# Optimization experiments

Hardware: AMD Instinct MI355X
Metric: run time of the kernel (lower is better)

The kernel has to match this reference:

```python
import jax, jax.numpy as jnp
from jax import lax
import numpy as np

EPS = 0.1          # DBSCAN radius (init arg eps)
MIN_SAMPLES = 5    # DBSCAN min_samples (init arg min_samples)
NC_MAX = 512       # fixed padded cluster budget (8 per dim * 64 dims)


def _dbscan_1d(x):
    """Exact 1-D DBSCAN on a vector x of shape (N,).
    Returns (labels, n_clusters). labels[i] in [-1, n_clusters), -1 = noise.
    Clusters are numbered in ascending value order (canonical deterministic
    relabeling of sklearn's discovery order). Border points are attached to
    the nearest core point (ties -> left)."""
    n = x.shape[0]
    order = jnp.argsort(x)
    xs = x[order]
    # core test: #points within [xs-eps, xs+eps] >= min_samples
    hi = jnp.searchsorted(xs, xs + EPS, side='right')
    lo = jnp.searchsorted(xs, xs - EPS, side='left')
    core = (hi - lo) >= MIN_SAMPLES
    inf = jnp.inf
    core_vals = jnp.where(core, xs, -inf)
    run_max = lax.cummax(core_vals, axis=0)                 # nearest core value to the left (incl self)
    prev_core_val = jnp.concatenate([jnp.full((1,), -inf, xs.dtype), run_max[:-1]])
    # a core point starts a new cluster iff no core point within eps on its left
    new_cluster = core & ((xs - prev_core_val) > EPS)
    starts = jnp.cumsum(new_cluster.astype(jnp.int32))
    cid = starts - 1                                        # cluster id carried along sorted order
    ncl = starts[-1]
    # nearest core on the left / right (values and their cluster ids)
    left_cid = lax.cummax(jnp.where(core, cid, -1), axis=0)
    left_val = run_max
    right_cid = lax.cummin(jnp.where(core, cid, n + 1), axis=0, reverse=True)
    right_val = lax.cummin(jnp.where(core, xs, inf), axis=0, reverse=True)
    dl = xs - left_val
    dr = right_val - xs
    border_cid = jnp.where(dl <= dr, left_cid, right_cid)
    border_ok = jnp.minimum(dl, dr) <= EPS
    lab_sorted = jnp.where(core, cid, jnp.where(border_ok, border_cid, -1))
    labels = jnp.zeros_like(lab_sorted).at[order].set(lab_sorted)  # unsort to original node order
    return labels, ncl


def setup_inputs() -> dict:
    key = jax.random.key(0)
    features = jax.random.normal(key, (8, 16384, 64), dtype=jnp.float32)
    return {"features": features}


def reference(features):
    B, N, D = features.shape
    xt = jnp.transpose(features, (0, 2, 1))                  # (B, D, N)
    labels, ncl = jax.vmap(jax.vmap(_dbscan_1d))(xt)         # (B, D, N), (B, D)
    off = jnp.cumsum(ncl, axis=1) - ncl                      # exclusive prefix: global cluster offset per dim
    glb = jnp.where(labels >= 0, labels + off[:, :, None], -1)
    # noise / overflow -> dump into padding column NC_MAX, sliced off below
    lbl = jnp.where(glb >= 0, jnp.minimum(glb, NC_MAX), NC_MAX)
    inc = jnp.zeros((B, N, NC_MAX + 1), features.dtype)
    b_ix = jnp.arange(B)[:, None, None]
    n_ix = jnp.arange(N)[None, None, :]
    inc = inc.at[b_ix, n_ix, lbl].set(1.0)                   # scatter cluster membership
    return inc[:, :, :NC_MAX]                                # (B, N, NC_MAX) padded incidence matrix
```

## Files before the change

kernel.cpp:

```cpp
#include <hip/hip_runtime.h>

#define NPTS   16384
#define NDIM   64
#define NBATCH 8
#define TB     1024
#define VPT    16
#define NB     8192
#define BPT    8
#define EPSF   0.1f
#define MINS   5
#define NCMAX  512
#define BIGI   0x3fffffff

__device__ __forceinline__ int phys(int i)  { return i ^ ((i >> 5) & 15); }
__device__ __forceinline__ int lphys(int i) { return i ^ (((i >> 6) & 31) << 1); }

__device__ __forceinline__ int binof(float x, float mn, float inv) {
  float fb = (x - mn) * inv;
  int b = (int)fb;
  if (fb < 0.f) b = 0;
  if (b > NB - 1) b = NB - 1;
  return b;
}

__global__ void ktrans(const float* __restrict__ f, float* __restrict__ xt) {
  __shared__ float tile[64][65];
  int blk = blockIdx.x;
  int b   = blk >> 8;
  int n0  = (blk & 255) << 6;
  for (int i = threadIdx.x; i < 64 * 64; i += 256) {
    int n = i >> 6, d = i & 63;
    tile[n][d] = f[((size_t)b * NPTS + n0 + n) * NDIM + d];
  }
  __syncthreads();
  for (int i = threadIdx.x; i < 64 * 64; i += 256) {
    int d = i >> 6, n = i & 63;
    xt[((size_t)b * NDIM + d) * NPTS + n0 + n] = tile[n][d];
  }
}

struct FS { int h; float f; float l; int li; int c; };
__device__ __forceinline__ FS fsid() { FS r; r.h = 0; r.f = 0.f; r.l = 0.f; r.li = -1; r.c = 0; return r; }
__device__ __forceinline__ FS fscomb(FS a, FS b) {
  FS r;
  r.h  = a.h | b.h;
  r.f  = a.h ? a.f : b.f;
  r.l  = b.h ? b.l : a.l;
  r.li = b.h ? b.li : a.li;
  int gap = (a.h && b.h && ((b.f - a.l) > EPSF)) ? 1 : 0;
  r.c  = a.c + b.c + gap;
  return r;
}

__global__ void __launch_bounds__(TB) kdbscan(const float* __restrict__ xt,
                                              short* __restrict__ labels,
                                              int* __restrict__ nclg) {
  const int tid  = threadIdx.x;
  const int lane = tid & 63;
  const int wid  = tid >> 6;
  const int bd   = blockIdx.x;
  const float* __restrict__ x = xt + (size_t)bd * NPTS;

  __shared__ float xs[NPTS];
  __shared__ unsigned int hist[NB];
  __shared__ unsigned int offs[NB];
  __shared__ float wmn[16], wmx[16];
  __shared__ unsigned int wsum[16];
  __shared__ int   sh[16];  __shared__ float sf[16], sl[16];
  __shared__ int   sli[16]; __shared__ int   sc[16];
  __shared__ int   wri[16]; __shared__ float wrv[16];
  short* lab = (short*)hist;

  float v[VPT];
  float mn = INFINITY, mx = -INFINITY;
  #pragma unroll
  for (int s = 0; s < VPT; ++s) {
    v[s] = x[tid + s * TB];
    mn = fminf(mn, v[s]); mx = fmaxf(mx, v[s]);
  }
  for (int d = 1; d < 64; d <<= 1) {
    mn = fminf(mn, __shfl_xor(mn, d));
    mx = fmaxf(mx, __shfl_xor(mx, d));
  }
  if (lane == 0) { wmn[wid] = mn; wmx[wid] = mx; }
  __syncthreads();
  mn = wmn[0]; mx = wmx[0];
  for (int w = 1; w < 16; ++w) { mn = fminf(mn, wmn[w]); mx = fmaxf(mx, wmx[w]); }
  float range = mx - mn;
  float inv = (range > 0.f) ? ((float)NB / range) : 0.f;

  for (int i = tid; i < NB; i += TB) hist[i] = 0u;
  __syncthreads();
  #pragma unroll
  for (int s = 0; s < VPT; ++s) atomicAdd(&hist[binof(v[s], mn, inv)], 1u);
  __syncthreads();

  unsigned int loc[BPT];
  unsigned int run = 0;
  const int bbase = tid * BPT;
  #pragma unroll
  for (int j = 0; j < BPT; ++j) { loc[j] = run; run += hist[bbase + j]; }
  unsigned int incl = run;
  for (int d = 1; d < 64; d <<= 1) {
    unsigned int u = __shfl_up(incl, d);
    if (lane >= d) incl += u;
  }
  unsigned int exc = __shfl_up(incl, 1);
  if (lane == 0) exc = 0u;
  if (lane == 63) wsum[wid] = incl;
  __syncthreads();
  unsigned int wb = 0;
  for (int w = 0; w < wid; ++w) wb += wsum[w];
  unsigned int tb0 = wb + exc;
  #pragma unroll
  for (int j = 0; j < BPT; ++j) offs[bbase + j] = tb0 + loc[j];
  __syncthreads();

  int pos[VPT];
  #pragma unroll
  for (int s = 0; s < VPT; ++s) {
    int b = binof(v[s], mn, inv);
    int p = (int)atomicAdd(&offs[b], 1u);
    pos[s] = p;
    xs[phys(p)] = v[s];
  }
  __syncthreads();

  int tgt[VPT];
  #pragma unroll
  for (int s = 0; s < VPT; ++s) {
    int b  = binof(v[s], mn, inv);
    int e0 = (int)offs[b];
    int s0 = e0 - (int)hist[b];
    float vv = v[s]; int pp = pos[s];
    int r = 0;
    for (int j = s0; j < e0; ++j) {
      float xj = xs[phys(j)];
      r += (xj < vv || (xj == vv && j < pp)) ? 1 : 0;
    }
    tgt[s] = s0 + r;
  }
  __syncthreads();
  #pragma unroll
  for (int s = 0; s < VPT; ++s) xs[phys(tgt[s])] = v[s];
  __syncthreads();

  const int p0 = tid * VPT;
  float w[VPT + 8];
  #pragma unroll
  for (int k = 0; k < VPT + 8; ++k) {
    int i = p0 - 4 + k;
    w[k] = (i < 0) ? -INFINITY : ((i >= NPTS) ? INFINITY : xs[phys(i)]);
  }
  unsigned int coremask = 0u;
  #pragma unroll
  for (int s = 0; s < VPT; ++s) {
    float xi = w[s + 4];
    float lo = xi - EPSF, hi = xi + EPSF;
    bool core = false;
    #pragma unroll
    for (int t = 0; t < MINS; ++t)
      core |= (w[s + 4 - t] >= lo) && (w[s + 8 - t] <= hi);
    if (core) coremask |= (1u << s);
  }

  FS ch = fsid();
  #pragma unroll
  for (int s = 0; s < VPT; ++s) {
    if ((coremask >> s) & 1u) {
      float xv = w[s + 4];
      if (!ch.h) { ch.h = 1; ch.f = xv; }
      else if ((xv - ch.l) > EPSF) ++ch.c;
      ch.l = xv; ch.li = p0 + s;
    }
  }
  FS cur = ch;
  for (int d = 1; d < 64; d <<= 1) {
    FS u;
    u.h  = __shfl_up(cur.h, d);
    u.f  = __shfl_up(cur.f, d);
    u.l  = __shfl_up(cur.l, d);
    u.li = __shfl_up(cur.li, d);
    u.c  = __shfl_up(cur.c, d);
    FS cmb = fscomb(u, cur);
    if (lane >= d) cur = cmb;
  }
  FS exs;
  exs.h  = __shfl_up(cur.h, 1);
  exs.f  = __shfl_up(cur.f, 1);
  exs.l  = __shfl_up(cur.l, 1);
  exs.li = __shfl_up(cur.li, 1);
  exs.c  = __shfl_up(cur.c, 1);
  if (lane == 0) exs = fsid();
  if (lane == 63) { sh[wid] = cur.h; sf[wid] = cur.f; sl[wid] = cur.l; sli[wid] = cur.li; sc[wid] = cur.c; }
  __syncthreads();
  FS pre = fsid();
  for (int w2 = 0; w2 < wid; ++w2) {
    FS t; t.h = sh[w2]; t.f = sf[w2]; t.l = sl[w2]; t.li = sli[w2]; t.c = sc[w2];
    pre = fscomb(pre, t);
  }
  FS sp = fscomb(pre, exs);

  float P  = sp.h ? sp.l  : -INFINITY;
  int   Pi = sp.h ? sp.li : -1;
  int starts = sp.h ? (sp.c + 1) : 0;
  int   li[VPT];
  float lv[VPT];
  #pragma unroll
  for (int s = 0; s < VPT; ++s) {
    int i = p0 + s;
    if ((coremask >> s) & 1u) {
      float xv = w[s + 4];
      if ((xv - P) > EPSF) ++starts;
      P = xv; Pi = i;
      lab[lphys(i)] = (short)(starts - 1);
    }
    li[s] = Pi; lv[s] = P;
  }
  if (tid == TB - 1) nclg[bd] = starts;

  int fi_ = BIGI; float fv_ = 0.f;
  #pragma unroll
  for (int s = VPT - 1; s >= 0; --s)
    if ((coremask >> s) & 1u) { fi_ = p0 + s; fv_ = w[s + 4]; }
  int ri = fi_; float rv = fv_;
  for (int d = 1; d < 64; d <<= 1) {
    int ui = __shfl_down(ri, d); float uv = __shfl_down(rv, d);
    if (lane < 64 - d && ui < ri) { ri = ui; rv = uv; }
  }
  int rei = __shfl_down(ri, 1); float rev = __shfl_down(rv, 1);
  if (lane == 63) rei = BIGI;
  if (lane == 0) { wri[wid] = ri; wrv[wid] = rv; }
  __syncthreads();
  int Ri = rei; float Rv = rev;
  for (int w2 = wid + 1; w2 < 16; ++w2)
    if (wri[w2] < Ri) { Ri = wri[w2]; Rv = wrv[w2]; }
  #pragma unroll
  for (int s = VPT - 1; s >= 0; --s) {
    int i = p0 + s;
    if ((coremask >> s) & 1u) { Ri = i; Rv = w[s + 4]; }
    else {
      float xi = w[s + 4];
      float dl = xi - lv[s];
      float dr = (Ri < NPTS) ? (Rv - xi) : INFINITY;
      short lb = -1;
      if (fminf(dl, dr) <= EPSF)
        lb = (dl <= dr) ? lab[lphys(li[s])] : lab[lphys(Ri)];
      lab[lphys(i)] = lb;
    }
  }
  __syncthreads();

  #pragma unroll
  for (int s = 0; s < VPT; ++s)
    labels[(size_t)bd * NPTS + tid + s * TB] = lab[lphys(tgt[s])];
}

__global__ void __launch_bounds__(TB) kout(const short* __restrict__ labels,
                                           const int* __restrict__ ncl,
                                           float* __restrict__ out) {
  const int tid  = threadIdx.x;
  const int lane = tid & 63;
  const int wid  = tid >> 6;
  const int b    = blockIdx.x >> 5;
  const int n0   = (blockIdx.x & 31) * 512 + wid * 32;

  __shared__ int cmLDS[NCMAX];
  for (int k = tid; k < NCMAX; k += TB) cmLDS[k] = -1;
  __syncthreads();
  if (tid < 64) {
    int vcnt = ncl[b * 64 + tid];
    int incl = vcnt;
    for (int d = 1; d < 64; d <<= 1) {
      int u = __shfl_up(incl, d);
      if (tid >= d) incl += u;
    }
    int off = incl - vcnt;
    for (int k = 0; k < vcnt; ++k) {
      int col = off + k;
      if (col < NCMAX) cmLDS[col] = tid | (k << 8);
    }
  }
  __syncthreads();

  int cm[8];
  #pragma unroll
  for (int k = 0; k < 8; ++k) {
    int col = (k < 4) ? (lane * 4 + k) : (256 + lane * 4 + (k - 4));
    cm[k] = cmLDS[col];
  }
  const short* lb_b = labels + (size_t)b * NDIM * NPTS;

  for (int r = 0; r < 32; ++r) {
    int n = n0 + r;
    float o[8];
    #pragma unroll
    for (int k = 0; k < 8; ++k) {
      int m = cm[k];
      float val = 0.f;
      if (m >= 0) {
        int d  = m & 255;
        int kk = m >> 8;
        val = (lb_b[(size_t)d * NPTS + n] == (short)kk) ? 1.0f : 0.0f;
      }
      o[k] = val;
    }
    float4* op = (float4*)(out + ((size_t)b * NPTS + n) * NCMAX);
    op[lane]      = make_float4(o[0], o[1], o[2], o[3]);
    op[64 + lane] = make_float4(o[4], o[5], o[6], o[7]);
  }
}

extern "C" void kernel_launch(void* const* d_in, const int* in_sizes, int n_in,
                              void* d_out, int out_size, void* d_ws, size_t ws_size,
                              hipStream_t stream) {
  const float* feat = (const float*)d_in[0];
  float* out = (float*)d_out;

  char* ws = (char*)d_ws;
  size_t xt_b   = (size_t)NBATCH * NPTS * NDIM * 4;
  size_t lbl_b  = (size_t)NBATCH * NPTS * NDIM * 2;
  float* xt     = (float*)ws;
  short* labels = (short*)(ws + xt_b);
  int*   ncl    = (int*)(ws + xt_b + lbl_b);

  ktrans  <<<NBATCH * (NPTS / 64), 256, 0, stream>>>(feat, xt);
  kdbscan <<<NBATCH * NDIM, TB, 0, stream>>>(xt, labels, ncl);
  kout    <<<NBATCH * 32, TB, 0, stream>>>(labels, ncl, out);
}
```

Baseline: 165.5 us.

## Vectorize label loads, use nontemporal output stores, and fuse DBSCAN labeling passes

The output kernel now loads eight consecutive labels per column with one 16-byte short8 load instead of one scalar short load per row. It writes the large incidence matrix with nontemporal stores to reduce cache pollution. In the DBSCAN kernel, the bin index is packed into pos so binof is not recomputed, the core-test and chain-summary loops are merged, and the li/index scan state is dropped. Border labels are now computed in a single forward pass using ctz to find the next core point, instead of reading back core labels from LDS.

```diff
diff --git a/kernel.cpp b/kernel.cpp
--- a/kernel.cpp
+++ b/kernel.cpp
@@ -12,6 +12,9 @@
 #define NCMAX  512
 #define BIGI   0x3fffffff
 
+typedef short short8 __attribute__((ext_vector_type(8)));
+typedef float f32x4  __attribute__((ext_vector_type(4)));
+
 __device__ __forceinline__ int phys(int i)  { return i ^ ((i >> 5) & 15); }
 __device__ __forceinline__ int lphys(int i) { return i ^ (((i >> 6) & 31) << 1); }
 
@@ -39,16 +42,15 @@
   }
 }
 
-struct FS { int h; float f; float l; int li; int c; };
-__device__ __forceinline__ FS fsid() { FS r; r.h = 0; r.f = 0.f; r.l = 0.f; r.li = -1; r.c = 0; return r; }
+struct FS { int h; float f; float l; int c; };
+__device__ __forceinline__ FS fsid() { FS r; r.h = 0; r.f = 0.f; r.l = 0.f; r.c = 0; return r; }
 __device__ __forceinline__ FS fscomb(FS a, FS b) {
   FS r;
-  r.h  = a.h | b.h;
-  r.f  = a.h ? a.f : b.f;
-  r.l  = b.h ? b.l : a.l;
-  r.li = b.h ? b.li : a.li;
+  r.h = a.h | b.h;
+  r.f = a.h ? a.f : b.f;
+  r.l = b.h ? b.l : a.l;
   int gap = (a.h && b.h && ((b.f - a.l) > EPSF)) ? 1 : 0;
-  r.c  = a.c + b.c + gap;
+  r.c = a.c + b.c + gap;
   return r;
 }
 
@@ -66,8 +68,7 @@
   __shared__ unsigned int offs[NB];
   __shared__ float wmn[16], wmx[16];
   __shared__ unsigned int wsum[16];
-  __shared__ int   sh[16];  __shared__ float sf[16], sl[16];
-  __shared__ int   sli[16]; __shared__ int   sc[16];
+  __shared__ int   sh[16];  __shared__ float sf[16], sl[16]; __shared__ int sc[16];
   __shared__ int   wri[16]; __shared__ float wrv[16];
   short* lab = (short*)hist;
 
@@ -121,7 +122,7 @@
   for (int s = 0; s < VPT; ++s) {
     int b = binof(v[s], mn, inv);
     int p = (int)atomicAdd(&offs[b], 1u);
-    pos[s] = p;
+    pos[s] = p | (b << 14);
     xs[phys(p)] = v[s];
   }
   __syncthreads();
@@ -129,10 +130,11 @@
   int tgt[VPT];
   #pragma unroll
   for (int s = 0; s < VPT; ++s) {
-    int b  = binof(v[s], mn, inv);
+    int b  = pos[s] >> 14;
+    int pp = pos[s] & 0x3FFF;
     int e0 = (int)offs[b];
     int s0 = e0 - (int)hist[b];
-    float vv = v[s]; int pp = pos[s];
+    float vv = v[s];
     int r = 0;
     for (int j = s0; j < e0; ++j) {
       float xj = xs[phys(j)];
@@ -141,6 +143,7 @@
     tgt[s] = s0 + r;
   }
   __syncthreads();
+
   #pragma unroll
   for (int s = 0; s < VPT; ++s) xs[phys(tgt[s])] = v[s];
   __syncthreads();
@@ -153,6 +156,8 @@
     w[k] = (i < 0) ? -INFINITY : ((i >= NPTS) ? INFINITY : xs[phys(i)]);
   }
   unsigned int coremask = 0u;
+  FS ch = fsid();
+  int fi = BIGI; float fv = 0.f;
   #pragma unroll
   for (int s = 0; s < VPT; ++s) {
     float xi = w[s + 4];
@@ -161,94 +166,78 @@
     #pragma unroll
     for (int t = 0; t < MINS; ++t)
       core |= (w[s + 4 - t] >= lo) && (w[s + 8 - t] <= hi);
-    if (core) coremask |= (1u << s);
-  }
-
-  FS ch = fsid();
-  #pragma unroll
-  for (int s = 0; s < VPT; ++s) {
-    if ((coremask >> s) & 1u) {
-      float xv = w[s + 4];
-      if (!ch.h) { ch.h = 1; ch.f = xv; }
-      else if ((xv - ch.l) > EPSF) ++ch.c;
-      ch.l = xv; ch.li = p0 + s;
-    }
-  }
+    if (core) {
+      coremask |= (1u << s);
+      if (!ch.h) { ch.h = 1; ch.f = xi; }
+      else if ((xi - ch.l) > EPSF) ++ch.c;
+      ch.l = xi;
+      if (fi == BIGI) { fi = p0 + s; fv = xi; }
+    }
+  }
+
   FS cur = ch;
   for (int d = 1; d < 64; d <<= 1) {
     FS u;
-    u.h  = __shfl_up(cur.h, d);
-    u.f  = __shfl_up(cur.f, d);
-    u.l  = __shfl_up(cur.l, d);
-    u.li = __shfl_up(cur.li, d);
-    u.c  = __shfl_up(cur.c, d);
+    u.h = __shfl_up(cur.h, d);
+    u.f = __shfl_up(cur.f, d);
+    u.l = __shfl_up(cur.l, d);
+    u.c = __shfl_up(cur.c, d);
     FS cmb = fscomb(u, cur);
     if (lane >= d) cur = cmb;
   }
   FS exs;
-  exs.h  = __shfl_up(cur.h, 1);
-  exs.f  = __shfl_up(cur.f, 1);
-  exs.l  = __shfl_up(cur.l, 1);
-  exs.li = __shfl_up(cur.li, 1);
-  exs.c  = __shfl_up(cur.c, 1);
+  exs.h = __shfl_up(cur.h, 1);
+  exs.f = __shfl_up(cur.f, 1);
+  exs.l = __shfl_up(cur.l, 1);
+  exs.c = __shfl_up(cur.c, 1);
   if (lane == 0) exs = fsid();
-  if (lane == 63) { sh[wid] = cur.h; sf[wid] = cur.f; sl[wid] = cur.l; sli[wid] = cur.li; sc[wid] = cur.c; }
+  if (lane == 63) { sh[wid] = cur.h; sf[wid] = cur.f; sl[wid] = cur.l; sc[wid] = cur.c; }
   __syncthreads();
   FS pre = fsid();
   for (int w2 = 0; w2 < wid; ++w2) {
-    FS t; t.h = sh[w2]; t.f = sf[w2]; t.l = sl[w2]; t.li = sli[w2]; t.c = sc[w2];
+    FS t; t.h = sh[w2]; t.f = sf[w2]; t.l = sl[w2]; t.c = sc[w2];
     pre = fscomb(pre, t);
   }
   FS sp = fscomb(pre, exs);
 
-  float P  = sp.h ? sp.l  : -INFINITY;
-  int   Pi = sp.h ? sp.li : -1;
-  int starts = sp.h ? (sp.c + 1) : 0;
-  int   li[VPT];
-  float lv[VPT];
-  #pragma unroll
-  for (int s = 0; s < VPT; ++s) {
-    int i = p0 + s;
-    if ((coremask >> s) & 1u) {
-      float xv = w[s + 4];
-      if ((xv - P) > EPSF) ++starts;
-      P = xv; Pi = i;
-      lab[lphys(i)] = (short)(starts - 1);
-    }
-    li[s] = Pi; lv[s] = P;
-  }
-  if (tid == TB - 1) nclg[bd] = starts;
-
-  int fi_ = BIGI; float fv_ = 0.f;
-  #pragma unroll
-  for (int s = VPT - 1; s >= 0; --s)
-    if ((coremask >> s) & 1u) { fi_ = p0 + s; fv_ = w[s + 4]; }
-  int ri = fi_; float rv = fv_;
+  int ri = fi; float rv = fv;
   for (int d = 1; d < 64; d <<= 1) {
     int ui = __shfl_down(ri, d); float uv = __shfl_down(rv, d);
     if (lane < 64 - d && ui < ri) { ri = ui; rv = uv; }
   }
-  int rei = __shfl_down(ri, 1); float rev = __shfl_down(rv, 1);
-  if (lane == 63) rei = BIGI;
+  int Ri = __shfl_down(ri, 1); float Rv = __shfl_down(rv, 1);
+  if (lane == 63) Ri = BIGI;
   if (lane == 0) { wri[wid] = ri; wrv[wid] = rv; }
   __syncthreads();
-  int Ri = rei; float Rv = rev;
   for (int w2 = wid + 1; w2 < 16; ++w2)
     if (wri[w2] < Ri) { Ri = wri[w2]; Rv = wrv[w2]; }
-  #pragma unroll
-  for (int s = VPT - 1; s >= 0; --s) {
+
+  float P  = sp.h ? sp.l : -INFINITY;
+  int starts = sp.h ? (sp.c + 1) : 0;
+  #pragma unroll
+  for (int s = 0; s < VPT; ++s) {
     int i = p0 + s;
-    if ((coremask >> s) & 1u) { Ri = i; Rv = w[s + 4]; }
-    else {
-      float xi = w[s + 4];
-      float dl = xi - lv[s];
-      float dr = (Ri < NPTS) ? (Rv - xi) : INFINITY;
-      short lb = -1;
+    float xi = w[s + 4];
+    short lb;
+    if ((coremask >> s) & 1u) {
+      if ((xi - P) > EPSF) ++starts;
+      P = xi;
+      lb = (short)(starts - 1);
+    } else {
+      float dl = xi - P;
+      unsigned hb = coremask >> (s + 1);
+      float Rv2; bool has;
+      if (hb) { int j = s + 1 + __builtin_ctz(hb); Rv2 = w[4 + j]; has = true; }
+      else    { Rv2 = Rv; has = (Ri < NPTS); }
+      float dr = has ? (Rv2 - xi) : INFINITY;
+      lb = -1;
       if (fminf(dl, dr) <= EPSF)
-        lb = (dl <= dr) ? lab[lphys(li[s])] : lab[lphys(Ri)];
-      lab[lphys(i)] = lb;
-    }
-  }
+        lb = (short)((dl <= dr) ? (starts - 1)
+                                : (starts - 1 + (((Rv2 - P) > EPSF) ? 1 : 0)));
+    }
+    lab[lphys(i)] = lb;
+  }
+  if (tid == TB - 1) nclg[bd] = starts;
   __syncthreads();
 
   #pragma unroll
@@ -283,31 +272,35 @@
   }
   __syncthreads();
 
-  int cm[8];
+  int dk[8], kk[8];
   #pragma unroll
   for (int k = 0; k < 8; ++k) {
     int col = (k < 4) ? (lane * 4 + k) : (256 + lane * 4 + (k - 4));
-    cm[k] = cmLDS[col];
+    int m = cmLDS[col];
+    dk[k] = (m >= 0) ? (m & 255) : 0;
+    kk[k] = (m >= 0) ? (m >> 8) : 0x7FFF;
   }
   const short* lb_b = labels + (size_t)b * NDIM * NPTS;
 
-  for (int r = 0; r < 32; ++r) {
-    int n = n0 + r;
-    float o[8];
+  #pragma unroll
+  for (int rc = 0; rc < 4; ++rc) {
+    short8 L[8];
     #pragma unroll
-    for (int k = 0; k < 8; ++k) {
-      int m = cm[k];
-      float val = 0.f;
-      if (m >= 0) {
-        int d  = m & 255;
-        int kk = m >> 8;
-        val = (lb_b[(size_t)d * NPTS + n] == (short)kk) ? 1.0f : 0.0f;
-      }
-      o[k] = val;
-    }
-    float4* op = (float4*)(out + ((size_t)b * NPTS + n) * NCMAX);
-    op[lane]      = make_float4(o[0], o[1], o[2], o[3]);
-    op[64 + lane] = make_float4(o[4], o[5], o[6], o[7]);
+    for (int k = 0; k < 8; ++k)
+      L[k] = *(const short8*)(lb_b + (size_t)dk[k] * NPTS + n0 + rc * 8);
+    #pragma unroll
+    for (int r2 = 0; r2 < 8; ++r2) {
+      int n = n0 + rc * 8 + r2;
+      float o[8];
+      #pragma unroll
+      for (int k = 0; k < 8; ++k)
+        o[k] = (L[k][r2] == (short)kk[k]) ? 1.0f : 0.0f;
+      f32x4* op = (f32x4*)(out + ((size_t)b * NPTS + n) * NCMAX);
+      f32x4 lo4 = { o[0], o[1], o[2], o[3] };
+      f32x4 hi4 = { o[4], o[5], o[6], o[7] };
+      __builtin_nontemporal_store(lo4, &op[lane]);
+      __builtin_nontemporal_store(hi4, &op[64 + lane]);
+    }
   }
 }
 
```

Measured after the change: 153.0 us. -7.6%, faster.
